# Performance work log

Hardware: AMD Instinct MI355X
Metric: run time of the kernel (lower is better)

Reference implementation:

```python
import jax, jax.numpy as jnp
import numpy as np

NUM_QUBITS = 8
QD = 2 ** NUM_QUBITS          # 256
PI = float(np.pi)
D_MODEL = 512
NUM_HEADS = 8
HEAD_DIM = D_MODEL // NUM_HEADS
LN_EPS = 1e-5


def _superposition(feat):
    # torch bug faithfully reproduced: state starts as e0 and is *multiplied*
    # by per-qubit amplitudes, so only index 0 survives. All values real.
    B, S, d = feat.shape
    idx = np.arange(NUM_QUBITS) % d
    theta = feat[:, :, idx] * PI                       # [B,S,nq]
    cos_h = jnp.cos(theta * 0.5)
    sin_h = jnp.sin(theta * 0.5)
    mask = (np.arange(QD)[None, :] >> np.arange(NUM_QUBITS)[:, None]) & 1  # [nq,QD]
    amps = jnp.where(mask[None, None] == 0, cos_h[..., None], sin_h[..., None])  # [B,S,nq,QD]
    prod = jnp.prod(amps, axis=2)                      # [B,S,QD]
    e0 = jnp.zeros((QD,), feat.dtype).at[0].set(1.0)
    state = prod * e0
    norm = jnp.sqrt(jnp.sum(state * state, axis=-1, keepdims=True))
    return state / (norm + 1e-10)


def _linear_entangle(ent):
    # entangle_matrix is block-diagonal with symmetric 2x2 blocks [[a,a],[a,-a]];
    # state @ M.T == pairwise 2x2 matmul (identical math, avoids 65536^2 matrix)
    B, S, D = ent.shape
    a = 0.7071
    M = jnp.array([[a, a], [a, -a]], ent.dtype)
    return (ent.reshape(B, S, D // 2, 2) @ M).reshape(B, S, D)


def _layer_norm(x, g, b):
    m = jnp.mean(x, axis=-1, keepdims=True)
    v = jnp.mean((x - m) ** 2, axis=-1, keepdims=True)
    return (x - m) * jax.lax.rsqrt(v + LN_EPS) * g + b


def setup_inputs() -> dict:
    key = jax.random.key(0)
    ks = jax.random.split(key, 16)
    D = D_MODEL
    s = 1.0 / np.sqrt(D)
    inp = {
        'audio_features': jax.random.normal(ks[0], (2, 256, D), jnp.float32),
        'visual_features': jax.random.normal(ks[1], (2, 256, D), jnp.float32),
        'Wq': jax.random.normal(ks[2], (D, D), jnp.float32) * s,
        'bq': jnp.zeros((D,), jnp.float32),
        'Wk': jax.random.normal(ks[3], (D, D), jnp.float32) * s,
        'bk': jnp.zeros((D,), jnp.float32),
        'Wv': jax.random.normal(ks[4], (D, D), jnp.float32) * s,
        'bv': jnp.zeros((D,), jnp.float32),
        'Wo': jax.random.normal(ks[5], (D, D), jnp.float32) * s,
        'bo': jnp.zeros((D,), jnp.float32),
        'We': jax.random.normal(ks[6], (D, D), jnp.float32) * s,
        'be': jnp.zeros((D,), jnp.float32),
        'gamma': jnp.ones((D,), jnp.float32),
        'beta': jnp.zeros((D,), jnp.float32),
    }
    return inp


def reference(audio_features, visual_features, Wq, bq, Wk, bk, Wv, bv,
              Wo, bo, We, be, gamma, beta):
    B, S, D = audio_features.shape
    H, hd = NUM_HEADS, HEAD_DIM

    aq = audio_features @ Wq + bq
    av = audio_features @ Wv + bv
    vk = visual_features @ Wk + bk
    vv = visual_features @ Wv + bv

    qa = _superposition(audio_features @ We + be)    # [B,S,QD]
    qv = _superposition(visual_features @ We + be)   # [B,S,QD]
    ent = (qa[..., :, None] * qv[..., None, :]).reshape(B, S, QD * QD)
    ent = _linear_entangle(ent)                      # [B,S,QD^2]

    probs = ent * ent
    qsum = jnp.sum(probs, axis=-1)                   # [B,S]
    ang = jnp.where(ent < 0, PI, 0.0)                # angle of a real number
    interference = jnp.cos(jnp.mean(ang, axis=-1))   # [B,S]
    scale = (qsum * interference)[:, None, :, None]  # [B,1,S,1]

    def heads(x):
        return x.reshape(B, S, H, hd).transpose(0, 2, 1, 3)

    aqh, vkh, vvh, avh = heads(aq), heads(vk), heads(vv), heads(av)
    logits = scale * jnp.einsum('bhqd,bhkd->bhqk', aqh, vkh) / np.sqrt(hd)
    attn = jax.nn.softmax(logits, axis=-1)           # [B,H,S,S]

    audio_att = jnp.einsum('bhqk,bhkd->bhqd', attn, vvh)
    visual_att = jnp.einsum('bhqk,bhqd->bhkd', attn, avh)
    audio_out = audio_att.transpose(0, 2, 1, 3).reshape(B, S, D) @ Wo + bo
    visual_out = visual_att.transpose(0, 2, 1, 3).reshape(B, S, D) @ Wo + bo

    audio_final = _layer_norm(audio_features + audio_out, gamma, beta)
    visual_final = _layer_norm(visual_features + visual_out, gamma, beta)

    quantum_coherence = jnp.mean(jnp.abs(ent))
    pn = probs / (jnp.sum(probs, axis=-1, keepdims=True) + 1e-10)
    entanglement_entropy = jnp.mean(-jnp.sum(pn * jnp.log(pn + 1e-10), axis=-1))

    return (audio_final, visual_final, quantum_coherence,
            entanglement_entropy, attn[:, -1])
```

## Files before the change

kernel.cpp:

```cpp
#include <hip/hip_runtime.h>
#include <math.h>

#define PI_F 3.14159265358979323846f

typedef __attribute__((ext_vector_type(8))) short short8v;
typedef __attribute__((ext_vector_type(4))) float f32x4;
typedef __attribute__((ext_vector_type(16))) float f32x16;

__device__ __forceinline__ unsigned short f2bf(float f) {
    unsigned int u = __float_as_uint(f);
    u += 0x7fffu + ((u >> 16) & 1u);
    return (unsigned short)(u >> 16);
}

__device__ __forceinline__ unsigned int cvtpk_bf16(float lo, float hi) {
    unsigned int r;
    asm("v_cvt_pk_bf16_f32 %0, %1, %2" : "=v"(r) : "v"(lo), "v"(hi));
    return r;
}

union W8 { unsigned int w[4]; short8v v; };

__device__ __forceinline__ void gload_lds16(const void* g, void* l) {
    __builtin_amdgcn_global_load_lds((const __attribute__((address_space(1))) unsigned int*)g,
                                     (__attribute__((address_space(3))) unsigned int*)l, 16, 0, 0);
}

__global__ __launch_bounds__(256) void prep_tok(const float* __restrict__ audio,
                                                const float* __restrict__ visual,
                                                const float* __restrict__ Wq,
                                                const float* __restrict__ Wk,
                                                const float* __restrict__ Wv,
                                                const float* __restrict__ Wo,
                                                const float* __restrict__ We,
                                                const float* __restrict__ be,
                                                unsigned short* __restrict__ audio_b,
                                                unsigned short* __restrict__ visual_b,
                                                unsigned short* __restrict__ Wqt,
                                                unsigned short* __restrict__ Wkt,
                                                unsigned short* __restrict__ Wvt,
                                                unsigned short* __restrict__ Wot,
                                                float* __restrict__ scale,
                                                float* __restrict__ coh_tok,
                                                float* __restrict__ ent_tok) {
    __shared__ float tile[32][33];
    const int bid = blockIdx.x;
    if (bid < 1536) {
        const int z = bid >> 8;
        const int x0 = (bid & 15) * 32, y0 = ((bid >> 4) & 15) * 32;
        const int tx = threadIdx.x & 31, ty = threadIdx.x >> 5;
        if (z < 2) {
            const float* src = z ? visual : audio;
            unsigned short* dst = z ? visual_b : audio_b;
#pragma unroll
            for (int i = 0; i < 4; i++) {
                int r = y0 + ty + i * 8;
                dst[r * 512 + x0 + tx] = f2bf(src[r * 512 + x0 + tx]);
            }
        } else {
            const float* src = (z == 2) ? Wq : (z == 3) ? Wk : (z == 4) ? Wv : Wo;
            unsigned short* dst = (z == 2) ? Wqt : (z == 3) ? Wkt : (z == 4) ? Wvt : Wot;
#pragma unroll
            for (int i = 0; i < 4; i++)
                tile[ty + i * 8][tx] = src[(y0 + ty + i * 8) * 512 + x0 + tx];
            __syncthreads();
#pragma unroll
            for (int i = 0; i < 4; i++) {
                int n = x0 + ty + i * 8;
                dst[n * 512 + y0 + tx] = f2bf(tile[tx][ty + i * 8]);
            }
        }
    } else {
        const int t = (bid - 1536) * 4 + (threadIdx.x >> 6);
        const int lane = threadIdx.x & 63;
        float accA[8] = {}, accV[8] = {};
#pragma unroll
        for (int i = 0; i < 8; i++) {
            int k = i * 64 + lane;
            float wa = audio[t * 512 + k], wv = visual[t * 512 + k];
            const float* wrow = &We[k * 512];
#pragma unroll
            for (int c = 0; c < 8; c++) {
                float w = wrow[c];
                accA[c] += wa * w;
                accV[c] += wv * w;
            }
        }
#pragma unroll
        for (int c = 0; c < 8; c++) {
#pragma unroll
            for (int o = 32; o >= 1; o >>= 1) {
                accA[c] += __shfl_xor(accA[c], o);
                accV[c] += __shfl_xor(accV[c], o);
            }
        }
        if (lane == 0) {
            float pa = 1.f, pv = 1.f;
#pragma unroll
            for (int c = 0; c < 8; c++) {
                pa *= cosf((accA[c] + be[c]) * (PI_F * 0.5f));
                pv *= cosf((accV[c] + be[c]) * (PI_F * 0.5f));
            }
            float s0a = pa / (fabsf(pa) + 1e-10f);
            float s0v = pv / (fabsf(pv) + 1e-10f);
            float e = s0a * s0v;
            const float a = 0.7071f;
            float ent0 = a * e;
            float qsum = 2.f * ent0 * ent0;
            float interf = (ent0 < 0.f) ? cosf(2.f * PI_F / 65536.f) : 1.f;
            scale[t] = qsum * interf;
            coh_tok[t] = 2.f * fabsf(ent0);
            float p = (ent0 * ent0) / (qsum + 1e-10f);
            ent_tok[t] = -2.f * p * logf(p + 1e-10f);
        }
    }
}

struct MfmaArgs {
    const unsigned short* A[4];
    const unsigned short* Bt[4];
    const float* bias[4];
    void* C[4];
    int obf[4];
    int otr[4];
};

__global__ __launch_bounds__(256) void gemm_mfma(MfmaArgs args) {
    const int zb = blockIdx.z;
    const unsigned short* __restrict__ A = args.A[zb];
    const unsigned short* __restrict__ Bt = args.Bt[zb];
    const float* __restrict__ bias = args.bias[zb];
    const int otr = args.otr[zb];

    const int n0 = blockIdx.x * 64;
    const int m0 = blockIdx.y * 64;

    __shared__ unsigned short As[64 * 64];
    __shared__ unsigned short Bs[64 * 64];

    const int tid = threadIdx.x;
    const int lane = tid & 63;
    const int wid = tid >> 6;
    const int wr = wid >> 1, wc = wid & 1;
    const int l15 = lane & 15;
    const int lhi = lane >> 4;

    f32x4 acc[2][2] = {};

    for (int kt = 0; kt < 8; kt++) {
        const int k0 = kt * 64;
#pragma unroll
        for (int i = 0; i < 2; i++) {
            int row = i * 32 + wid * 8 + (lane >> 3);
            int pc = lane & 7;
            int lc = pc ^ (row & 7);
            const unsigned short* gA = A + (m0 + row) * 512 + k0 + lc * 8;
            const unsigned short* gB = Bt + (n0 + row) * 512 + k0 + lc * 8;
            gload_lds16(gA, (char*)As + i * 4096 + wid * 1024);
            gload_lds16(gB, (char*)Bs + i * 4096 + wid * 1024);
        }
        __syncthreads();
#pragma unroll
        for (int ks = 0; ks < 2; ks++) {
            short8v a[2], b[2];
            const int lcr = ks * 4 + lhi;
#pragma unroll
            for (int qi = 0; qi < 2; qi++) {
                int row = wr * 32 + qi * 16 + l15;
                int pcc = lcr ^ (row & 7);
                a[qi] = *(const short8v*)((const char*)As + row * 128 + pcc * 16);
            }
#pragma unroll
            for (int nj = 0; nj < 2; nj++) {
                int row = wc * 32 + nj * 16 + l15;
                int pcc = lcr ^ (row & 7);
                b[nj] = *(const short8v*)((const char*)Bs + row * 128 + pcc * 16);
            }
            if (otr) {
#pragma unroll
                for (int qi = 0; qi < 2; qi++)
#pragma unroll
                    for (int nj = 0; nj < 2; nj++)
                        acc[qi][nj] = __builtin_amdgcn_mfma_f32_16x16x32_bf16(b[nj], a[qi], acc[qi][nj], 0, 0, 0);
            } else {
#pragma unroll
                for (int qi = 0; qi < 2; qi++)
#pragma unroll
                    for (int nj = 0; nj < 2; nj++)
                        acc[qi][nj] = __builtin_amdgcn_mfma_f32_16x16x32_bf16(a[qi], b[nj], acc[qi][nj], 0, 0, 0);
            }
        }
        __syncthreads();
    }

    if (otr) {
        unsigned short* __restrict__ Ct = (unsigned short*)args.C[zb];
#pragma unroll
        for (int qi = 0; qi < 2; qi++)
#pragma unroll
            for (int nj = 0; nj < 2; nj++)
#pragma unroll
                for (int r = 0; r < 4; r++) {
                    int nrow = n0 + wc * 32 + nj * 16 + lhi * 4 + r;
                    int tcol = m0 + wr * 32 + qi * 16 + l15;
                    Ct[nrow * 512 + tcol] = f2bf(acc[qi][nj][r] + bias[nrow]);
                }
    } else if (args.obf[zb]) {
        unsigned short* __restrict__ Cb = (unsigned short*)args.C[zb];
#pragma unroll
        for (int qi = 0; qi < 2; qi++)
#pragma unroll
            for (int nj = 0; nj < 2; nj++)
#pragma unroll
                for (int r = 0; r < 4; r++) {
                    int row = m0 + wr * 32 + qi * 16 + lhi * 4 + r;
                    int col = n0 + wc * 32 + nj * 16 + l15;
                    Cb[row * 512 + col] = f2bf(acc[qi][nj][r] + bias[col]);
                }
    } else {
        float* __restrict__ C = (float*)args.C[zb];
#pragma unroll
        for (int qi = 0; qi < 2; qi++)
#pragma unroll
            for (int nj = 0; nj < 2; nj++)
#pragma unroll
                for (int r = 0; r < 4; r++) {
                    int row = m0 + wr * 32 + qi * 16 + lhi * 4 + r;
                    int col = n0 + wc * 32 + nj * 16 + l15;
                    C[row * 512 + col] = acc[qi][nj][r] + bias[col];
                }
    }
}

__global__ __launch_bounds__(512, 2) void attn_roles(const unsigned short* __restrict__ aqb,
                                                     const unsigned short* __restrict__ vkb,
                                                     const unsigned short* __restrict__ vvt,
                                                     const unsigned short* __restrict__ avt,
                                                     const float* __restrict__ scale,
                                                     const float* __restrict__ coh,
                                                     const float* __restrict__ entt,
                                                     unsigned short* __restrict__ attcat_b,
                                                     float* __restrict__ attn_last,
                                                     float* __restrict__ scal_out) {
    __shared__ char smem[65536];
    char* Kb = smem;
    char* VF = smem + 32768;

    const int tid = threadIdx.x;
    const int wid = tid >> 6;
    const int lane = tid & 63;
    const int lq = lane & 31;
    const int hi = lane >> 5;

    if (blockIdx.x == 8) {
        if (blockIdx.y || blockIdx.z) return;
        float c = coh[tid], e = entt[tid];
#pragma unroll
        for (int o = 32; o >= 1; o >>= 1) {
            c += __shfl_xor(c, o);
            e += __shfl_xor(e, o);
        }
        float* rc = (float*)smem;
        float* re = rc + 8;
        if (lane == 0) { rc[wid] = c; re[wid] = e; }
        __syncthreads();
        if (tid == 0) {
            float cs = 0.f, es = 0.f;
#pragma unroll
            for (int i = 0; i < 8; i++) { cs += rc[i]; es += re[i]; }
            scal_out[0] = cs / (512.f * 65536.f);
            scal_out[1] = es / 512.f;
        }
        return;
    }

    const int h = blockIdx.x, b = blockIdx.y, role = blockIdx.z;

    {
#pragma unroll
        for (int i = 0; i < 4; i++) {
            int r = wid * 32 + i * 8 + (lane >> 3);
            int lc = (lane & 7) ^ (r & 7);
            gload_lds16(vkb + (size_t)(b * 256 + r) * 512 + h * 64 + lc * 8,
                        Kb + wid * 4096 + i * 1024);
        }
    }

    if (role == 0) {
#pragma unroll
        for (int i = 0; i < 4; i++) {
            gload_lds16(vvt + (size_t)(h * 64 + 32 * hi + lq) * 512 + b * 256 + 32 * wid + 8 * i,
                        VF + wid * 4096 + i * 1024);
        }
    }
    __syncthreads();

    f32x16 p[8] = {};
    {
        short8v qf[4];
        const unsigned short* qbase = aqb + (size_t)(b * 256 + wid * 32 + lq) * 512 + h * 64;
#pragma unroll
        for (int s = 0; s < 4; s++) qf[s] = *(const short8v*)(qbase + (2 * s + hi) * 8);
#pragma unroll
        for (int t = 0; t < 8; t++) {
            const int krow = t * 32 + lq;
#pragma unroll
            for (int s = 0; s < 4; s++) {
                int slot = (2 * s + hi) ^ (krow & 7);
                short8v kf = *(const short8v*)(Kb + krow * 128 + (slot << 4));
                p[t] = __builtin_amdgcn_mfma_f32_32x32x16_bf16(kf, qf[s], p[t], 0, 0, 0);
            }
        }
    }

    {
        const float sq = scale[b * 256 + wid * 32 + lq] * 0.125f;
        float mx = -1e30f;
#pragma unroll
        for (int t = 0; t < 8; t++) {
            p[t] *= sq;
#pragma unroll
            for (int r = 0; r < 16; r++) mx = fmaxf(mx, p[t][r]);
        }
        mx = fmaxf(mx, __shfl_xor(mx, 32));
        float sum = 0.f;
#pragma unroll
        for (int t = 0; t < 8; t++)
#pragma unroll
            for (int r = 0; r < 16; r++) {
                float e = __expf(p[t][r] - mx);
                p[t][r] = e;
                sum += e;
            }
        sum += __shfl_xor(sum, 32);
        float inv = 1.0f / sum;
#pragma unroll
        for (int t = 0; t < 8; t++) p[t] *= inv;
    }

    if (role == 0) {
        f32x16 aacc[2] = {};
#pragma unroll
        for (int t = 0; t < 8; t++) {
            unsigned int c0 = cvtpk_bf16(p[t][0], p[t][1]);
            unsigned int c1 = cvtpk_bf16(p[t][2], p[t][3]);
            unsigned int c2 = cvtpk_bf16(p[t][4], p[t][5]);
            unsigned int c3 = cvtpk_bf16(p[t][6], p[t][7]);
            unsigned int e0 = (unsigned int)__shfl_xor((int)c0, 32);
            unsigned int e1 = (unsigned int)__shfl_xor((int)c1, 32);
            unsigned int e2 = (unsigned int)__shfl_xor((int)c2, 32);
            unsigned int e3 = (unsigned int)__shfl_xor((int)c3, 32);
            W8 fa0;
            fa0.w[0] = hi ? e2 : c0;
            fa0.w[1] = hi ? e3 : c1;
            fa0.w[2] = hi ? c2 : e0;
            fa0.w[3] = hi ? c3 : e1;
            unsigned int c4 = cvtpk_bf16(p[t][8], p[t][9]);
            unsigned int c5 = cvtpk_bf16(p[t][10], p[t][11]);
            unsigned int c6 = cvtpk_bf16(p[t][12], p[t][13]);
            unsigned int c7 = cvtpk_bf16(p[t][14], p[t][15]);
            unsigned int e4 = (unsigned int)__shfl_xor((int)c4, 32);
            unsigned int e5 = (unsigned int)__shfl_xor((int)c5, 32);
            unsigned int e6 = (unsigned int)__shfl_xor((int)c6, 32);
            unsigned int e7 = (unsigned int)__shfl_xor((int)c7, 32);
            W8 fa1;
            fa1.w[0] = hi ? e6 : c4;
            fa1.w[1] = hi ? e7 : c5;
            fa1.w[2] = hi ? c6 : e4;
            fa1.w[3] = hi ? c7 : e5;
#pragma unroll
            for (int dt = 0; dt < 2; dt++) {
                short8v vf = *(const short8v*)(VF + ((((t * 4 + hi) * 2 + dt) * 32 + lq) << 4));
                aacc[dt] = __builtin_amdgcn_mfma_f32_32x32x16_bf16(fa0.v, vf, aacc[dt], 0, 0, 0);
                short8v vg = *(const short8v*)(VF + ((((t * 4 + hi + 2) * 2 + dt) * 32 + lq) << 4));
                aacc[dt] = __builtin_amdgcn_mfma_f32_32x32x16_bf16(fa1.v, vg, aacc[dt], 0, 0, 0);
            }
        }
#pragma unroll
        for (int dt = 0; dt < 2; dt++)
#pragma unroll
            for (int r = 0; r < 16; r++) {
                int qrow = wid * 32 + (r & 3) + 8 * (r >> 2) + 4 * hi;
                attcat_b[(size_t)(b * 256 + qrow) * 512 + h * 64 + 32 * dt + lq] = f2bf(aacc[dt][r]);
            }
        __syncthreads();

        if (h == 7) {
            float* tile = (float*)smem + (size_t)wid * (32 * 33);
            const int q2 = lane >> 1, koff = (lane & 1) * 16;
#pragma unroll
            for (int t = 0; t < 8; t++) {
#pragma unroll
                for (int r = 0; r < 16; r++)
                    tile[lq * 33 + ((r & 3) + 8 * (r >> 2) + 4 * hi)] = p[t][r];
                __syncthreads();
                float* orow = attn_last + (size_t)(b * 256 + wid * 32 + q2) * 256 + 32 * t + koff;
#pragma unroll
                for (int j = 0; j < 16; j++) orow[j] = tile[q2 * 33 + koff + j];
                __syncthreads();
            }
        }
        return;
    }

    __syncthreads();

    {
#pragma unroll
        for (int i = 0; i < 4; i++) {
            gload_lds16(avt + (size_t)(h * 64 + 32 * hi + lq) * 512 + b * 256 + 8 * (wid * 4 + i),
                        Kb + wid * 4096 + i * 1024);
        }
        if ((wid >> 1) == 0) {
            const int dq = (wid & 1) * 32 + lq;
#pragma unroll
            for (int t = 0; t < 8; t++)
#pragma unroll
                for (int r = 0; r < 16; r++) {
                    int k = 32 * t + (r & 3) + 8 * (r >> 2) + 4 * hi;
                    int slot = (dq >> 3) ^ ((k ^ (k >> 3)) & 7);
                    *(unsigned short*)(VF + k * 128 + slot * 16 + (dq & 7) * 2) = f2bf(p[t][r]);
                }
        }
    }
    __syncthreads();

    f32x16 vacc[2] = {};
    {
        const int krow = wid * 32 + lq;
        const int xr = (krow ^ (krow >> 3)) & 7;
#pragma unroll
        for (int c = 0; c < 4; c++) {
#pragma unroll
            for (int uc = 0; uc < 4; uc++) {
                int slot = (2 * uc + hi) ^ xr;
                short8v pa = *(const short8v*)(VF + krow * 128 + slot * 16);
                int m = 2 * (4 * c + uc) + hi;
#pragma unroll
                for (int dt = 0; dt < 2; dt++) {
                    short8v af = *(const short8v*)(Kb + (((m * 2 + dt) * 32 + lq) << 4));
                    vacc[dt] = __builtin_amdgcn_mfma_f32_32x32x16_bf16(pa, af, vacc[dt], 0, 0, 0);
                }
            }
            if (c < 3) {
                __syncthreads();
                if ((wid >> 1) == c + 1) {
                    const int dq = (wid & 1) * 32 + lq;
#pragma unroll
                    for (int t = 0; t < 8; t++)
#pragma unroll
                        for (int r = 0; r < 16; r++) {
                            int k = 32 * t + (r & 3) + 8 * (r >> 2) + 4 * hi;
                            int slot = (dq >> 3) ^ ((k ^ (k >> 3)) & 7);
                            *(unsigned short*)(VF + k * 128 + slot * 16 + (dq & 7) * 2) = f2bf(p[t][r]);
                        }
                }
                __syncthreads();
            }
        }
    }
#pragma unroll
    for (int dt = 0; dt < 2; dt++)
#pragma unroll
        for (int r = 0; r < 16; r++) {
            int krow = wid * 32 + (r & 3) + 8 * (r >> 2) + 4 * hi;
            attcat_b[(size_t)(512 + b * 256 + krow) * 512 + h * 64 + 32 * dt + lq] = f2bf(vacc[dt][r]);
        }
}

__global__ __launch_bounds__(256) void ln_final(const float* __restrict__ xa,
                                                const float* __restrict__ xv,
                                                const float* __restrict__ proj,
                                                const float* __restrict__ gamma,
                                                const float* __restrict__ beta,
                                                float* __restrict__ out) {
    __shared__ float red[4];
    const int t = blockIdx.x;
    const int tid = threadIdx.x;
    const int wid = tid >> 6, lane = tid & 63;

    const float* x = (t < 512) ? (xa + t * 512) : (xv + (t - 512) * 512);
    const float* pp = proj + t * 512;

    float y0 = x[tid] + pp[tid];
    float y1 = x[tid + 256] + pp[tid + 256];

    float s = y0 + y1;
#pragma unroll
    for (int o = 32; o >= 1; o >>= 1) s += __shfl_xor(s, o);
    if (lane == 0) red[wid] = s;
    __syncthreads();
    float mean = (red[0] + red[1] + red[2] + red[3]) * (1.f / 512.f);

    float d0 = y0 - mean, d1 = y1 - mean;
    float v = d0 * d0 + d1 * d1;
    __syncthreads();
#pragma unroll
    for (int o = 32; o >= 1; o >>= 1) v += __shfl_xor(v, o);
    if (lane == 0) red[wid] = v;
    __syncthreads();
    float var = (red[0] + red[1] + red[2] + red[3]) * (1.f / 512.f);
    float rstd = rsqrtf(var + 1e-5f);

    out[t * 512 + tid] = d0 * rstd * gamma[tid] + beta[tid];
    out[t * 512 + tid + 256] = d1 * rstd * gamma[tid + 256] + beta[tid + 256];
}

extern "C" void kernel_launch(void* const* d_in, const int* in_sizes, int n_in,
                              void* d_out, int out_size, void* d_ws, size_t ws_size,
                              hipStream_t stream) {
    const float* audio  = (const float*)d_in[0];
    const float* visual = (const float*)d_in[1];
    const float* Wq = (const float*)d_in[2];
    const float* bq = (const float*)d_in[3];
    const float* Wk = (const float*)d_in[4];
    const float* bk = (const float*)d_in[5];
    const float* Wv = (const float*)d_in[6];
    const float* bv = (const float*)d_in[7];
    const float* Wo = (const float*)d_in[8];
    const float* bo = (const float*)d_in[9];
    const float* We = (const float*)d_in[10];
    const float* be = (const float*)d_in[11];
    const float* gamma = (const float*)d_in[12];
    const float* beta  = (const float*)d_in[13];
    float* out = (float*)d_out;

    float* ws = (float*)d_ws;
    float* proj  = ws;
    float* scale = ws + 524288;
    float* coh   = ws + 524800;
    float* entt  = ws + 525312;
    unsigned short* attcat_b = (unsigned short*)(ws + 525824);
    unsigned short* audio_b  = (unsigned short*)(ws + 787968);
    unsigned short* visual_b = (unsigned short*)(ws + 919040);
    unsigned short* Wqt  = (unsigned short*)(ws + 1050112);
    unsigned short* Wkt  = (unsigned short*)(ws + 1181184);
    unsigned short* Wvt  = (unsigned short*)(ws + 1312256);
    unsigned short* Wot  = (unsigned short*)(ws + 1443328);
    unsigned short* aq_b = (unsigned short*)(ws + 1574400);
    unsigned short* vk_b = (unsigned short*)(ws + 1705472);
    unsigned short* vvt  = (unsigned short*)(ws + 1836544);
    unsigned short* avt  = (unsigned short*)(ws + 1967616);

    hipLaunchKernelGGL(prep_tok, dim3(1664), dim3(256), 0, stream,
                       audio, visual, Wq, Wk, Wv, Wo, We, be,
                       audio_b, visual_b, Wqt, Wkt, Wvt, Wot,
                       scale, coh, entt);

    MfmaArgs g1;
    g1.A[0] = audio_b;  g1.Bt[0] = Wqt; g1.bias[0] = bq; g1.C[0] = aq_b; g1.obf[0] = 1; g1.otr[0] = 0;
    g1.A[1] = visual_b; g1.Bt[1] = Wkt; g1.bias[1] = bk; g1.C[1] = vk_b; g1.obf[1] = 1; g1.otr[1] = 0;
    g1.A[2] = visual_b; g1.Bt[2] = Wvt; g1.bias[2] = bv; g1.C[2] = vvt;  g1.obf[2] = 1; g1.otr[2] = 1;
    g1.A[3] = audio_b;  g1.Bt[3] = Wvt; g1.bias[3] = bv; g1.C[3] = avt;  g1.obf[3] = 1; g1.otr[3] = 1;
    hipLaunchKernelGGL(gemm_mfma, dim3(8, 8, 4), dim3(256), 0, stream, g1);

    hipLaunchKernelGGL(attn_roles, dim3(9, 2, 2), dim3(512), 0, stream,
                       aq_b, vk_b, vvt, avt, scale, coh, entt,
                       attcat_b, out + 524290, out + 524288);

    MfmaArgs g2;
    for (int i = 0; i < 4; i++) {
        g2.A[i] = attcat_b; g2.Bt[i] = Wot; g2.bias[i] = bo; g2.C[i] = proj;
        g2.obf[i] = 0; g2.otr[i] = 0;
    }
    hipLaunchKernelGGL(gemm_mfma, dim3(8, 16, 1), dim3(256), 0, stream, g2);

    hipLaunchKernelGGL(ln_final, dim3(1024), dim3(256), 0, stream,
                       audio, visual, proj, gamma, beta, out);
}
```

Baseline: 52.35 us.

## Fuse output projection GEMM with residual add and LayerNorm

Replaces the separate output-projection GEMM and LayerNorm kernels with a single kernel. Each block computes a full 64-row by 512-column tile of the projection and then applies bias, residual and LayerNorm in registers. This removes a launch and the fp32 intermediate write and read. The grid shrinks to 16 blocks, leaving most compute units idle and serializing the K loop with no load/compute overlap.

```diff
diff --git a/kernel.cpp b/kernel.cpp
--- a/kernel.cpp
+++ b/kernel.cpp
@@ -468,42 +468,121 @@
         }
 }
 
-__global__ __launch_bounds__(256) void ln_final(const float* __restrict__ xa,
-                                                const float* __restrict__ xv,
-                                                const float* __restrict__ proj,
-                                                const float* __restrict__ gamma,
-                                                const float* __restrict__ beta,
-                                                float* __restrict__ out) {
-    __shared__ float red[4];
-    const int t = blockIdx.x;
+__global__ __launch_bounds__(256, 1) void gemm2_ln(const unsigned short* __restrict__ A,
+                                                   const unsigned short* __restrict__ Bt,
+                                                   const float* __restrict__ bias,
+                                                   const float* __restrict__ audio,
+                                                   const float* __restrict__ visual,
+                                                   const float* __restrict__ gamma,
+                                                   const float* __restrict__ beta,
+                                                   float* __restrict__ out) {
+    __shared__ unsigned short As[64 * 64];
+    __shared__ unsigned short Bs[256 * 64];
+    __shared__ float gb[512 * 3];
+
+    const int m0 = blockIdx.x * 64;
     const int tid = threadIdx.x;
-    const int wid = tid >> 6, lane = tid & 63;
-
-    const float* x = (t < 512) ? (xa + t * 512) : (xv + (t - 512) * 512);
-    const float* pp = proj + t * 512;
-
-    float y0 = x[tid] + pp[tid];
-    float y1 = x[tid + 256] + pp[tid + 256];
-
-    float s = y0 + y1;
-#pragma unroll
-    for (int o = 32; o >= 1; o >>= 1) s += __shfl_xor(s, o);
-    if (lane == 0) red[wid] = s;
-    __syncthreads();
-    float mean = (red[0] + red[1] + red[2] + red[3]) * (1.f / 512.f);
-
-    float d0 = y0 - mean, d1 = y1 - mean;
-    float v = d0 * d0 + d1 * d1;
-    __syncthreads();
-#pragma unroll
-    for (int o = 32; o >= 1; o >>= 1) v += __shfl_xor(v, o);
-    if (lane == 0) red[wid] = v;
-    __syncthreads();
-    float var = (red[0] + red[1] + red[2] + red[3]) * (1.f / 512.f);
-    float rstd = rsqrtf(var + 1e-5f);
-
-    out[t * 512 + tid] = d0 * rstd * gamma[tid] + beta[tid];
-    out[t * 512 + tid + 256] = d1 * rstd * gamma[tid + 256] + beta[tid + 256];
+    const int lane = tid & 63;
+    const int wid = tid >> 6;
+    const int l15 = lane & 15;
+    const int lhi = lane >> 4;
+
+    for (int i = tid; i < 512; i += 256) {
+        gb[i] = gamma[i];
+        gb[512 + i] = beta[i];
+        gb[1024 + i] = bias[i];
+    }
+
+    f32x4 acc[2][16] = {};
+
+#pragma unroll
+    for (int h = 0; h < 2; h++) {
+        for (int kt = 0; kt < 8; kt++) {
+            const int k0 = kt * 64;
+#pragma unroll
+            for (int i = 0; i < 2; i++) {
+                int row = i * 32 + wid * 8 + (lane >> 3);
+                int lc = (lane & 7) ^ (row & 7);
+                gload_lds16(A + (size_t)(m0 + row) * 512 + k0 + lc * 8,
+                            (char*)As + i * 4096 + wid * 1024);
+            }
+#pragma unroll
+            for (int i = 0; i < 8; i++) {
+                int row = wid * 64 + i * 8 + (lane >> 3);
+                int lc = (lane & 7) ^ (row & 7);
+                gload_lds16(Bt + (size_t)(h * 256 + row) * 512 + k0 + lc * 8,
+                            (char*)Bs + wid * 8192 + i * 1024);
+            }
+            __syncthreads();
+#pragma unroll
+            for (int ks = 0; ks < 2; ks++) {
+                const int lcr = ks * 4 + lhi;
+                const int arow = wid * 16 + l15;
+                short8v a = *(const short8v*)((const char*)As + arow * 128 + ((lcr ^ (arow & 7)) << 4));
+#pragma unroll
+                for (int nt = 0; nt < 16; nt++) {
+                    int brow = nt * 16 + l15;
+                    short8v b = *(const short8v*)((const char*)Bs + brow * 128 + ((lcr ^ (brow & 7)) << 4));
+                    acc[h][nt] = __builtin_amdgcn_mfma_f32_16x16x32_bf16(a, b, acc[h][nt], 0, 0, 0);
+                }
+            }
+            __syncthreads();
+        }
+    }
+
+    const float* xbase = (m0 < 512) ? (audio + (size_t)m0 * 512) : (visual + (size_t)(m0 - 512) * 512);
+#pragma unroll
+    for (int h = 0; h < 2; h++)
+#pragma unroll
+        for (int nt = 0; nt < 16; nt++) {
+            int col = h * 256 + nt * 16 + l15;
+            float bc = gb[1024 + col];
+#pragma unroll
+            for (int r = 0; r < 4; r++) {
+                int lrow = wid * 16 + lhi * 4 + r;
+                acc[h][nt][r] += bc + xbase[(size_t)lrow * 512 + col];
+            }
+        }
+
+    float mean[4], rstd[4];
+#pragma unroll
+    for (int r = 0; r < 4; r++) {
+        float s = 0.f;
+#pragma unroll
+        for (int h = 0; h < 2; h++)
+#pragma unroll
+            for (int nt = 0; nt < 16; nt++) s += acc[h][nt][r];
+#pragma unroll
+        for (int o = 1; o < 16; o <<= 1) s += __shfl_xor(s, o);
+        mean[r] = s * (1.f / 512.f);
+    }
+#pragma unroll
+    for (int r = 0; r < 4; r++) {
+        float v = 0.f;
+#pragma unroll
+        for (int h = 0; h < 2; h++)
+#pragma unroll
+            for (int nt = 0; nt < 16; nt++) {
+                float d = acc[h][nt][r] - mean[r];
+                v += d * d;
+            }
+#pragma unroll
+        for (int o = 1; o < 16; o <<= 1) v += __shfl_xor(v, o);
+        rstd[r] = rsqrtf(v * (1.f / 512.f) + 1e-5f);
+    }
+
+#pragma unroll
+    for (int h = 0; h < 2; h++)
+#pragma unroll
+        for (int nt = 0; nt < 16; nt++) {
+            int col = h * 256 + nt * 16 + l15;
+            float g = gb[col], bb = gb[512 + col];
+#pragma unroll
+            for (int r = 0; r < 4; r++) {
+                int row = m0 + wid * 16 + lhi * 4 + r;
+                out[(size_t)row * 512 + col] = (acc[h][nt][r] - mean[r]) * rstd[r] * g + bb;
+            }
+        }
 }
 
 extern "C" void kernel_launch(void* const* d_in, const int* in_sizes, int n_in,
@@ -526,21 +605,20 @@
     float* out = (float*)d_out;
 
     float* ws = (float*)d_ws;
-    float* proj  = ws;
-    float* scale = ws + 524288;
-    float* coh   = ws + 524800;
-    float* entt  = ws + 525312;
-    unsigned short* attcat_b = (unsigned short*)(ws + 525824);
-    unsigned short* audio_b  = (unsigned short*)(ws + 787968);
-    unsigned short* visual_b = (unsigned short*)(ws + 919040);
-    unsigned short* Wqt  = (unsigned short*)(ws + 1050112);
-    unsigned short* Wkt  = (unsigned short*)(ws + 1181184);
-    unsigned short* Wvt  = (unsigned short*)(ws + 1312256);
-    unsigned short* Wot  = (unsigned short*)(ws + 1443328);
-    unsigned short* aq_b = (unsigned short*)(ws + 1574400);
-    unsigned short* vk_b = (unsigned short*)(ws + 1705472);
-    unsigned short* vvt  = (unsigned short*)(ws + 1836544);
-    unsigned short* avt  = (unsigned short*)(ws + 1967616);
+    float* scale = ws;
+    float* coh   = ws + 512;
+    float* entt  = ws + 1024;
+    unsigned short* attcat_b = (unsigned short*)(ws + 1536);
+    unsigned short* audio_b  = (unsigned short*)(ws + 263680);
+    unsigned short* visual_b = (unsigned short*)(ws + 394752);
+    unsigned short* Wqt  = (unsigned short*)(ws + 525824);
+    unsigned short* Wkt  = (unsigned short*)(ws + 656896);
+    unsigned short* Wvt  = (unsigned short*)(ws + 787968);
+    unsigned short* Wot  = (unsigned short*)(ws + 919040);
+    unsigned short* aq_b = (unsigned short*)(ws + 1050112);
+    unsigned short* vk_b = (unsigned short*)(ws + 1181184);
+    unsigned short* vvt  = (unsigned short*)(ws + 1312256);
+    unsigned short* avt  = (unsigned short*)(ws + 1443328);
 
     hipLaunchKernelGGL(prep_tok, dim3(1664), dim3(256), 0, stream,
                        audio, visual, Wq, Wk, Wv, Wo, We, be,
@@ -558,13 +636,6 @@
                        aq_b, vk_b, vvt, avt, scale, coh, entt,
                        attcat_b, out + 524290, out + 524288);
 
-    MfmaArgs g2;
-    for (int i = 0; i < 4; i++) {
-        g2.A[i] = attcat_b; g2.Bt[i] = Wot; g2.bias[i] = bo; g2.C[i] = proj;
-        g2.obf[i] = 0; g2.otr[i] = 0;
-    }
-    hipLaunchKernelGGL(gemm_mfma, dim3(8, 16, 1), dim3(256), 0, stream, g2);
-
-    hipLaunchKernelGGL(ln_final, dim3(1024), dim3(256), 0, stream,
-                       audio, visual, proj, gamma, beta, out);
-}
+    hipLaunchKernelGGL(gemm2_ln, dim3(16), dim3(256), 0, stream,
+                       attcat_b, Wot, bo, audio, visual, gamma, beta, out);
+}
```

Measured after the change: 69.75 us. 33.2% more time.
